# Kernel tuning notes

Measured on AMD Instinct MI355X. Metric: run time of the kernel, lower is better.

Reference implementation:

```python
import jax, jax.numpy as jnp
import numpy as np

B, C, H, W = 8, 64, 64, 64
PROJ = 8


def setup_inputs() -> dict:
    key = jax.random.key(0)
    ks = jax.random.split(key, 8)
    inp = {
        "query_x": jax.random.normal(ks[0], (B, C, H, W), dtype=jnp.float32),
        "ref_x": jax.random.normal(ks[1], (B, C, H, W), dtype=jnp.float32),
        # 1x1 conv weights stored as [out_ch, in_ch] (kernel_size=1)
        "wq": jax.random.normal(ks[2], (PROJ, C), dtype=jnp.float32) * 0.05,
        "bq": jnp.zeros((PROJ,), dtype=jnp.float32),
        "wk": jax.random.normal(ks[3], (PROJ, C), dtype=jnp.float32) * 0.05,
        "bk": jnp.zeros((PROJ,), dtype=jnp.float32),
        "wv": jax.random.normal(ks[4], (C, C), dtype=jnp.float32) * 0.05,
        "bv": jnp.zeros((C,), dtype=jnp.float32),
    }
    return inp


def reference(query_x, ref_x, wq, bq, wk, bk, wv, bv):
    b, c, h, w = ref_x.shape
    n = h * w
    # 1x1 conv projections, flattened to [B, ch, HW]
    q = (jnp.einsum("oc,bchw->bohw", wq, query_x) + bq[None, :, None, None]).reshape(b, PROJ, n)
    k = (jnp.einsum("oc,bchw->bohw", wk, ref_x) + bk[None, :, None, None]).reshape(b, PROJ, n)
    v = (jnp.einsum("oc,bchw->bohw", wv, ref_x) + bv[None, :, None, None]).reshape(b, c, n)
    # energy[b, j(ref), i(query)] = sum_p k[b,p,j] * q[b,p,i]  (unscaled)
    energy = jnp.einsum("bpj,bpi->bji", k, q)
    attention = jax.nn.softmax(energy, axis=-1)
    # z = bmm(v, attention^T): z[b,c,j] = sum_i v[b,c,i] * attention[b,j,i]
    z = jnp.einsum("bci,bji->bcj", v, attention).reshape(b, c, h, w)
    return query_x + z
```

## Files before the change

### kernel.cpp

```cpp
#include <hip/hip_runtime.h>
#include <hip/hip_bf16.h>

#define B_ 8
#define C_ 64
#define N_ 4096
#define ITERS 16

typedef __attribute__((ext_vector_type(4))) short bf16x4;
typedef __attribute__((ext_vector_type(8))) short bf16x8;
typedef __attribute__((ext_vector_type(2))) float f32x2;
typedef __attribute__((ext_vector_type(4))) float f32x4;

static __device__ inline ushort f2bf(float x) {
    union { float f; unsigned u; } c; c.f = x;
    return (ushort)((c.u + 0x7FFFu + ((c.u >> 16) & 1u)) >> 16);
}
static __device__ inline float exp2fast(float x) {
#if __has_builtin(__builtin_amdgcn_exp2f)
    return __builtin_amdgcn_exp2f(x);
#else
    return exp2f(x);
#endif
}

#if __has_builtin(__builtin_amdgcn_mfma_f32_16x16x16bf16_1k)
static __device__ inline f32x4 mfma16(bf16x4 a, bf16x4 b, f32x4 c) {
    return __builtin_amdgcn_mfma_f32_16x16x16bf16_1k(a, b, c, 0, 0, 0);
}
#else
static __device__ inline f32x4 mfma16(bf16x4 a, bf16x4 b, f32x4 c) {
    bf16x8 a8 = (bf16x8){a[0], a[1], a[2], a[3], 0, 0, 0, 0};
    bf16x8 b8 = (bf16x8){b[0], b[1], b[2], b[3], 0, 0, 0, 0};
    return __builtin_amdgcn_mfma_f32_16x16x32_bf16(a8, b8, c, 0, 0, 0);
}
#endif
static __device__ inline f32x4 mfma32(bf16x8 a, bf16x8 b, f32x4 c) {
    return __builtin_amdgcn_mfma_f32_16x16x32_bf16(a, b, c, 0, 0, 0);
}

static __device__ inline void gload16(const void* g, void* l) {
#if __has_builtin(__builtin_amdgcn_global_load_lds)
    __builtin_amdgcn_global_load_lds(
        (const __attribute__((address_space(1))) void*)g,
        (__attribute__((address_space(3))) void*)l, 16, 0, 0);
#else
    const int lane = threadIdx.x & 63;
    *(int4*)((char*)l + lane * 16) = *(const int4*)((const char*)g + lane * 16);
#endif
}

__global__ __launch_bounds__(256) void proj_kernel(
    const float* __restrict__ qx, const float* __restrict__ rx,
    const float* __restrict__ wq, const float* __restrict__ bq,
    const float* __restrict__ wk, const float* __restrict__ bk,
    const float* __restrict__ wv, const float* __restrict__ bv,
    ushort* __restrict__ qb, ushort* __restrict__ kb, ushort* __restrict__ vt2)
{
    const int og  = blockIdx.y;
    const int gid = blockIdx.x * 256 + threadIdx.x;
    const int b   = gid >> 12;
    const int i   = gid & (N_ - 1);

    const int t  = i >> 5;
    const int lo = i & 7;
    const int hi = (i >> 3) & 3;
    ushort* tb = vt2 + ((size_t)(b * 128 + t)) * 2048;

    if (og == 0) {
        const float* xp = qx + (size_t)b * C_ * N_ + i;
        float a[8];
#pragma unroll
        for (int p = 0; p < 8; ++p) a[p] = bq[p];
        for (int c = 0; c < C_; ++c) {
            const float x = xp[(size_t)c * N_];
#pragma unroll
            for (int p = 0; p < 8; ++p) a[p] = fmaf(wq[p * C_ + c], x, a[p]);
        }
        ushort u8[8];
#pragma unroll
        for (int p = 0; p < 8; ++p) u8[p] = f2bf(a[p]);
        int4 r;
        r.x = (int)(u8[0] | ((unsigned)u8[1] << 16));
        r.y = (int)(u8[2] | ((unsigned)u8[3] << 16));
        r.z = (int)(u8[4] | ((unsigned)u8[5] << 16));
        r.w = (int)(u8[6] | ((unsigned)u8[7] << 16));
        *(int4*)(qb + (size_t)gid * 8) = r;
    } else if (og == 1) {
        const float* xp = rx + (size_t)b * C_ * N_ + i;
        float ak[8], av[32];
#pragma unroll
        for (int p = 0; p < 8; ++p) ak[p] = bk[p];
#pragma unroll
        for (int p = 0; p < 32; ++p) av[p] = bv[p];
        for (int c = 0; c < C_; ++c) {
            const float x = xp[(size_t)c * N_];
#pragma unroll
            for (int p = 0; p < 8; ++p) ak[p] = fmaf(wk[p * C_ + c], x, ak[p]);
#pragma unroll
            for (int p = 0; p < 32; ++p) av[p] = fmaf(wv[p * C_ + c], x, av[p]);
        }
        const float s = 1.44269504088896340736f;
        ushort u8[8];
#pragma unroll
        for (int p = 0; p < 8; ++p) u8[p] = f2bf(ak[p] * s);
        int4 r;
        r.x = (int)(u8[0] | ((unsigned)u8[1] << 16));
        r.y = (int)(u8[2] | ((unsigned)u8[3] << 16));
        r.z = (int)(u8[4] | ((unsigned)u8[5] << 16));
        r.w = (int)(u8[6] | ((unsigned)u8[7] << 16));
        *(int4*)(kb + (size_t)gid * 8) = r;
#pragma unroll
        for (int p = 0; p < 32; ++p)
            tb[p * 32 + ((hi ^ ((p >> 1) & 3)) << 3) + lo] = f2bf(av[p]);
    } else {
        const float* xp = rx + (size_t)b * C_ * N_ + i;
        float av[32];
#pragma unroll
        for (int p = 0; p < 32; ++p) av[p] = bv[32 + p];
        for (int c = 0; c < C_; ++c) {
            const float x = xp[(size_t)c * N_];
#pragma unroll
            for (int p = 0; p < 32; ++p)
                av[p] = fmaf(wv[(32 + p) * C_ + c], x, av[p]);
        }
#pragma unroll
        for (int p = 0; p < 32; ++p) {
            const int c = 32 + p;
            tb[c * 32 + ((hi ^ ((c >> 1) & 3)) << 3) + lo] = f2bf(av[p]);
        }
    }
}

__global__ __launch_bounds__(512, 4) void attn_kernel(
    const ushort* __restrict__ qb, const ushort* __restrict__ kb,
    const ushort* __restrict__ vt2, const float* __restrict__ qx,
    float* __restrict__ out)
{
    __shared__ __align__(16) char smem[65536];
    float* o_lds    = (float*)smem;
    float* lsum_lds = (float*)(smem + 2 * 64 * 68 * 4);

    const int tid  = threadIdx.x;
    const int ig   = tid >> 6;
    const int lane = tid & 63;
    const int cc   = lane & 15;
    const int g    = lane >> 4;
    const int b    = blockIdx.x;
    const int j0   = blockIdx.y * 64;

    bf16x4 bk[4];
#pragma unroll
    for (int jb = 0; jb < 4; ++jb) bk[jb] = (bf16x4){0, 0, 0, 0};
    if (g < 2) {
#pragma unroll
        for (int jb = 0; jb < 4; ++jb)
            bk[jb] = *(const bf16x4*)(kb + ((size_t)b * N_ + j0 + jb * 16 + cc) * 8 + g * 4);
    }

    const int qperm = 8 * (cc >> 2) + (cc & 3);
    const ushort* qptr = qb + ((size_t)b * N_ + (size_t)ig * (N_ / 8) + qperm) * 8 + g * 4;

    const char* vsl = (const char*)vt2 + ((size_t)(b * 128 + ig * 16)) * 4096 + lane * 16;
    char* lds0 = smem + ig * 8192;

    f32x4 acc[4][4];
#pragma unroll
    for (int jb = 0; jb < 4; ++jb)
#pragma unroll
        for (int ct = 0; ct < 4; ++ct) acc[jb][ct] = (f32x4){0.f, 0.f, 0.f, 0.f};
    f32x2 ls2[4];
#pragma unroll
    for (int jb = 0; jb < 4; ++jb) ls2[jb] = (f32x2){0.f, 0.f};
    const f32x4 zero4 = (f32x4){0.f, 0.f, 0.f, 0.f};

    const int rb = cc * 32 + ((g ^ ((cc >> 1) & 3)) << 3);

    bf16x4 qa0 = *(const bf16x4*)(qptr);
    bf16x4 qa1 = *(const bf16x4*)(qptr + 32);
    gload16(vsl, lds0);
    gload16(vsl + 1024, lds0 + 1024);
    gload16(vsl + 2048, lds0 + 2048);
    gload16(vsl + 3072, lds0 + 3072);
    bf16x4 qb0 = *(const bf16x4*)(qptr + 256);
    bf16x4 qb1 = *(const bf16x4*)(qptr + 256 + 32);
    asm volatile("s_waitcnt vmcnt(0)" ::: "memory");
    __builtin_amdgcn_sched_barrier(0);

#define HALF_ITER(Q0, Q1, RBOFF, WBOFF, IT)                                    \
    {                                                                          \
        asm volatile("s_waitcnt vmcnt(2)" ::: "memory");                       \
        __builtin_amdgcn_sched_barrier(0);                                     \
        const ushort* vtile = (const ushort*)(lds0 + (RBOFF));                 \
        bf16x8 av0 = *(const bf16x8*)(vtile + rb);                             \
        bf16x8 av1 = *(const bf16x8*)(vtile + rb + 512);                       \
        bf16x8 av2 = *(const bf16x8*)(vtile + rb + 1024);                      \
        bf16x8 av3 = *(const bf16x8*)(vtile + rb + 1536);                      \
        {                                                                      \
            const int nxt = ((IT) + 1) & (ITERS - 1);                          \
            const char* s = vsl + (size_t)nxt * 4096;                          \
            char* dd = lds0 + (WBOFF);                                         \
            gload16(s, dd);                                                    \
            gload16(s + 1024, dd + 1024);                                      \
            gload16(s + 2048, dd + 2048);                                      \
            gload16(s + 3072, dd + 3072);                                      \
        }                                                                      \
        __builtin_amdgcn_sched_barrier(0);                                     \
        _Pragma("unroll")                                                      \
        for (int jb = 0; jb < 4; ++jb) {                                       \
            f32x4 e0 = mfma16(Q0, bk[jb], zero4);                              \
            f32x4 e1 = mfma16(Q1, bk[jb], zero4);                              \
            float p0 = exp2fast(e0[0]), p1 = exp2fast(e0[1]);                  \
            float p2 = exp2fast(e0[2]), p3 = exp2fast(e0[3]);                  \
            float p4 = exp2fast(e1[0]), p5 = exp2fast(e1[1]);                  \
            float p6 = exp2fast(e1[2]), p7 = exp2fast(e1[3]);                  \
            union { bf16x8 v; __hip_bfloat162 h[4]; } pu;                      \
            pu.h[0] = __float22bfloat162_rn(make_float2(p0, p1));              \
            pu.h[1] = __float22bfloat162_rn(make_float2(p2, p3));              \
            pu.h[2] = __float22bfloat162_rn(make_float2(p4, p5));              \
            pu.h[3] = __float22bfloat162_rn(make_float2(p6, p7));              \
            f32x2 sA = (f32x2){p0, p1} + (f32x2){p2, p3};                      \
            f32x2 sB = (f32x2){p4, p5} + (f32x2){p6, p7};                      \
            ls2[jb] += sA + sB;                                                \
            acc[jb][0] = mfma32(av0, pu.v, acc[jb][0]);                        \
            acc[jb][1] = mfma32(av1, pu.v, acc[jb][1]);                        \
            acc[jb][2] = mfma32(av2, pu.v, acc[jb][2]);                        \
            acc[jb][3] = mfma32(av3, pu.v, acc[jb][3]);                        \
        }                                                                      \
        {                                                                      \
            const int nq = ((IT) + 2) & (ITERS - 1);                           \
            const ushort* qp = qptr + (size_t)nq * 256;                        \
            Q0 = *(const bf16x4*)(qp);                                         \
            Q1 = *(const bf16x4*)(qp + 32);                                    \
        }                                                                      \
    }

#pragma unroll 1
    for (int d = 0; d < ITERS / 2; ++d) {
        const int it0 = 2 * d;
        HALF_ITER(qa0, qa1, 0, 4096, it0);
        HALF_ITER(qb0, qb1, 4096, 0, it0 + 1);
    }
#undef HALF_ITER

    float ls[4];
#pragma unroll
    for (int jb = 0; jb < 4; ++jb) {
        ls[jb] = ls2[jb][0] + ls2[jb][1];
        ls[jb] += __shfl_xor(ls[jb], 16, 64);
        ls[jb] += __shfl_xor(ls[jb], 32, 64);
    }

    __syncthreads();
    {
        const int phme = ig >> 1;
        float* od = o_lds + (ig & 1) * (64 * 68);
        float* ld = lsum_lds + (ig & 1) * 64;
#pragma unroll 1
        for (int ph = 0; ph < 4; ++ph) {
            if (phme == ph) {
                if (ph == 0) {
#pragma unroll
                    for (int jb = 0; jb < 4; ++jb)
#pragma unroll
                        for (int ct = 0; ct < 4; ++ct)
#pragma unroll
                            for (int r = 0; r < 4; ++r)
                                od[(ct * 16 + 4 * g + r) * 68 + jb * 16 + cc] = acc[jb][ct][r];
                    if (g == 0) {
#pragma unroll
                        for (int jb = 0; jb < 4; ++jb) ld[jb * 16 + cc] = ls[jb];
                    }
                } else {
#pragma unroll
                    for (int jb = 0; jb < 4; ++jb)
#pragma unroll
                        for (int ct = 0; ct < 4; ++ct)
#pragma unroll
                            for (int r = 0; r < 4; ++r)
                                od[(ct * 16 + 4 * g + r) * 68 + jb * 16 + cc] += acc[jb][ct][r];
                    if (g == 0) {
#pragma unroll
                        for (int jb = 0; jb < 4; ++jb) ld[jb * 16 + cc] += ls[jb];
                    }
                }
            }
            __syncthreads();
        }
    }

    const int ec = tid >> 3;
    const int ej = (tid & 7) * 8;
    const float* xp = qx  + ((size_t)b * C_ + ec) * N_ + j0 + ej;
    float*       op = out + ((size_t)b * C_ + ec) * N_ + j0 + ej;
    float4 x0 = *(const float4*)xp;
    float4 x1 = *(const float4*)(xp + 4);
    float rr[8];
#pragma unroll
    for (int t = 0; t < 8; ++t) {
        const float num = o_lds[ec * 68 + ej + t] + o_lds[64 * 68 + ec * 68 + ej + t];
        const float den = lsum_lds[ej + t] + lsum_lds[64 + ej + t];
        rr[t] = num / den;
    }
    float4 r0 = make_float4(x0.x + rr[0], x0.y + rr[1], x0.z + rr[2], x0.w + rr[3]);
    float4 r1 = make_float4(x1.x + rr[4], x1.y + rr[5], x1.z + rr[6], x1.w + rr[7]);
    *(float4*)op       = r0;
    *(float4*)(op + 4) = r1;
}

extern "C" void kernel_launch(void* const* d_in, const int* in_sizes, int n_in,
                              void* d_out, int out_size, void* d_ws, size_t ws_size,
                              hipStream_t stream) {
    const float* qx = (const float*)d_in[0];
    const float* rx = (const float*)d_in[1];
    const float* wq = (const float*)d_in[2];
    const float* bq = (const float*)d_in[3];
    const float* wk = (const float*)d_in[4];
    const float* bk = (const float*)d_in[5];
    const float* wv = (const float*)d_in[6];
    const float* bv = (const float*)d_in[7];
    float* out = (float*)d_out;

    ushort* qb  = (ushort*)d_ws;
    ushort* kb  = qb + (size_t)B_ * N_ * 8;
    ushort* vt2 = kb + (size_t)B_ * N_ * 8;

    proj_kernel<<<dim3((B_ * N_) / 256, 3), 256, 0, stream>>>(
        qx, rx, wq, bq, wk, bk, wv, bv, qb, kb, vt2);

    attn_kernel<<<dim3(B_, N_ / 64), 512, 0, stream>>>(qb, kb, vt2, qx, out);
}
```

Before: 52.57 us.

## Load V fragments directly from global into registers, dropping LDS staging

The projection kernel now writes V in an MFMA-fragment-ready layout, so each lane can read its bf16x8 A-operands for the attention kernel straight from global memory. This removes the global_load_lds double-buffered staging, the manual vmcnt waits, the sched barriers and the LDS reads. It also shrinks shared memory to just the reduction buffers, which may allow more resident blocks. In exchange, register-prefetched global loads depend on the compiler to hide latency, without explicit pipeline control.

```diff
diff --git a/kernel.cpp b/kernel.cpp
--- a/kernel.cpp
+++ b/kernel.cpp
@@ -8,7 +8,6 @@
 
 typedef __attribute__((ext_vector_type(4))) short bf16x4;
 typedef __attribute__((ext_vector_type(8))) short bf16x8;
-typedef __attribute__((ext_vector_type(2))) float f32x2;
 typedef __attribute__((ext_vector_type(4))) float f32x4;
 
 static __device__ inline ushort f2bf(float x) {
@@ -36,17 +35,6 @@
 #endif
 static __device__ inline f32x4 mfma32(bf16x8 a, bf16x8 b, f32x4 c) {
     return __builtin_amdgcn_mfma_f32_16x16x32_bf16(a, b, c, 0, 0, 0);
-}
-
-static __device__ inline void gload16(const void* g, void* l) {
-#if __has_builtin(__builtin_amdgcn_global_load_lds)
-    __builtin_amdgcn_global_load_lds(
-        (const __attribute__((address_space(1))) void*)g,
-        (__attribute__((address_space(3))) void*)l, 16, 0, 0);
-#else
-    const int lane = threadIdx.x & 63;
-    *(int4*)((char*)l + lane * 16) = *(const int4*)((const char*)g + lane * 16);
-#endif
 }
 
 __global__ __launch_bounds__(256) void proj_kernel(
@@ -62,9 +50,10 @@
     const int i   = gid & (N_ - 1);
 
     const int t  = i >> 5;
-    const int lo = i & 7;
-    const int hi = (i >> 3) & 3;
-    ushort* tb = vt2 + ((size_t)(b * 128 + t)) * 2048;
+    const int il = i & 31;
+    const int fl = (il >> 3) * 16;
+    const int fe = il & 7;
+    ushort* tb = vt2 + (size_t)(b * 128 + t) * 2048;
 
     if (og == 0) {
         const float* xp = qx + (size_t)b * C_ * N_ + i;
@@ -111,7 +100,7 @@
         *(int4*)(kb + (size_t)gid * 8) = r;
 #pragma unroll
         for (int p = 0; p < 32; ++p)
-            tb[p * 32 + ((hi ^ ((p >> 1) & 3)) << 3) + lo] = f2bf(av[p]);
+            tb[(p >> 4) * 512 + (fl + (p & 15)) * 8 + fe] = f2bf(av[p]);
     } else {
         const float* xp = rx + (size_t)b * C_ * N_ + i;
         float av[32];
@@ -126,7 +115,7 @@
 #pragma unroll
         for (int p = 0; p < 32; ++p) {
             const int c = 32 + p;
-            tb[c * 32 + ((hi ^ ((c >> 1) & 3)) << 3) + lo] = f2bf(av[p]);
+            tb[(c >> 4) * 512 + (fl + (c & 15)) * 8 + fe] = f2bf(av[p]);
         }
     }
 }
@@ -136,9 +125,8 @@
     const ushort* __restrict__ vt2, const float* __restrict__ qx,
     float* __restrict__ out)
 {
-    __shared__ __align__(16) char smem[65536];
-    float* o_lds    = (float*)smem;
-    float* lsum_lds = (float*)(smem + 2 * 64 * 68 * 4);
+    __shared__ float o_lds[2 * 64 * 68];
+    __shared__ float lsum_lds[2 * 64];
 
     const int tid  = threadIdx.x;
     const int ig   = tid >> 6;
@@ -160,92 +148,61 @@
     const int qperm = 8 * (cc >> 2) + (cc & 3);
     const ushort* qptr = qb + ((size_t)b * N_ + (size_t)ig * (N_ / 8) + qperm) * 8 + g * 4;
 
-    const char* vsl = (const char*)vt2 + ((size_t)(b * 128 + ig * 16)) * 4096 + lane * 16;
-    char* lds0 = smem + ig * 8192;
+    const ushort* vbase = vt2 + (size_t)(b * 128 + ig * 16) * 2048 + lane * 8;
 
     f32x4 acc[4][4];
 #pragma unroll
     for (int jb = 0; jb < 4; ++jb)
 #pragma unroll
         for (int ct = 0; ct < 4; ++ct) acc[jb][ct] = (f32x4){0.f, 0.f, 0.f, 0.f};
-    f32x2 ls2[4];
-#pragma unroll
-    for (int jb = 0; jb < 4; ++jb) ls2[jb] = (f32x2){0.f, 0.f};
+    float ls[4] = {0.f, 0.f, 0.f, 0.f};
     const f32x4 zero4 = (f32x4){0.f, 0.f, 0.f, 0.f};
 
-    const int rb = cc * 32 + ((g ^ ((cc >> 1) & 3)) << 3);
-
+    bf16x8 av0 = *(const bf16x8*)(vbase);
+    bf16x8 av1 = *(const bf16x8*)(vbase + 512);
+    bf16x8 av2 = *(const bf16x8*)(vbase + 1024);
+    bf16x8 av3 = *(const bf16x8*)(vbase + 1536);
     bf16x4 qa0 = *(const bf16x4*)(qptr);
     bf16x4 qa1 = *(const bf16x4*)(qptr + 32);
-    gload16(vsl, lds0);
-    gload16(vsl + 1024, lds0 + 1024);
-    gload16(vsl + 2048, lds0 + 2048);
-    gload16(vsl + 3072, lds0 + 3072);
-    bf16x4 qb0 = *(const bf16x4*)(qptr + 256);
-    bf16x4 qb1 = *(const bf16x4*)(qptr + 256 + 32);
-    asm volatile("s_waitcnt vmcnt(0)" ::: "memory");
-    __builtin_amdgcn_sched_barrier(0);
-
-#define HALF_ITER(Q0, Q1, RBOFF, WBOFF, IT)                                    \
-    {                                                                          \
-        asm volatile("s_waitcnt vmcnt(2)" ::: "memory");                       \
-        __builtin_amdgcn_sched_barrier(0);                                     \
-        const ushort* vtile = (const ushort*)(lds0 + (RBOFF));                 \
-        bf16x8 av0 = *(const bf16x8*)(vtile + rb);                             \
-        bf16x8 av1 = *(const bf16x8*)(vtile + rb + 512);                       \
-        bf16x8 av2 = *(const bf16x8*)(vtile + rb + 1024);                      \
-        bf16x8 av3 = *(const bf16x8*)(vtile + rb + 1536);                      \
-        {                                                                      \
-            const int nxt = ((IT) + 1) & (ITERS - 1);                          \
-            const char* s = vsl + (size_t)nxt * 4096;                          \
-            char* dd = lds0 + (WBOFF);                                         \
-            gload16(s, dd);                                                    \
-            gload16(s + 1024, dd + 1024);                                      \
-            gload16(s + 2048, dd + 2048);                                      \
-            gload16(s + 3072, dd + 3072);                                      \
-        }                                                                      \
-        __builtin_amdgcn_sched_barrier(0);                                     \
-        _Pragma("unroll")                                                      \
-        for (int jb = 0; jb < 4; ++jb) {                                       \
-            f32x4 e0 = mfma16(Q0, bk[jb], zero4);                              \
-            f32x4 e1 = mfma16(Q1, bk[jb], zero4);                              \
-            float p0 = exp2fast(e0[0]), p1 = exp2fast(e0[1]);                  \
-            float p2 = exp2fast(e0[2]), p3 = exp2fast(e0[3]);                  \
-            float p4 = exp2fast(e1[0]), p5 = exp2fast(e1[1]);                  \
-            float p6 = exp2fast(e1[2]), p7 = exp2fast(e1[3]);                  \
-            union { bf16x8 v; __hip_bfloat162 h[4]; } pu;                      \
-            pu.h[0] = __float22bfloat162_rn(make_float2(p0, p1));              \
-            pu.h[1] = __float22bfloat162_rn(make_float2(p2, p3));              \
-            pu.h[2] = __float22bfloat162_rn(make_float2(p4, p5));              \
-            pu.h[3] = __float22bfloat162_rn(make_float2(p6, p7));              \
-            f32x2 sA = (f32x2){p0, p1} + (f32x2){p2, p3};                      \
-            f32x2 sB = (f32x2){p4, p5} + (f32x2){p6, p7};                      \
-            ls2[jb] += sA + sB;                                                \
-            acc[jb][0] = mfma32(av0, pu.v, acc[jb][0]);                        \
-            acc[jb][1] = mfma32(av1, pu.v, acc[jb][1]);                        \
-            acc[jb][2] = mfma32(av2, pu.v, acc[jb][2]);                        \
-            acc[jb][3] = mfma32(av3, pu.v, acc[jb][3]);                        \
-        }                                                                      \
-        {                                                                      \
-            const int nq = ((IT) + 2) & (ITERS - 1);                           \
-            const ushort* qp = qptr + (size_t)nq * 256;                        \
-            Q0 = *(const bf16x4*)(qp);                                         \
-            Q1 = *(const bf16x4*)(qp + 32);                                    \
-        }                                                                      \
-    }
-
-#pragma unroll 1
-    for (int d = 0; d < ITERS / 2; ++d) {
-        const int it0 = 2 * d;
-        HALF_ITER(qa0, qa1, 0, 4096, it0);
-        HALF_ITER(qb0, qb1, 4096, 0, it0 + 1);
-    }
-#undef HALF_ITER
-
-    float ls[4];
+
+#pragma unroll 2
+    for (int it = 0; it < ITERS; ++it) {
+        const int nxt = (it + 1) & (ITERS - 1);
+        const ushort* vp = vbase + nxt * 2048;
+        bf16x8 nv0 = *(const bf16x8*)(vp);
+        bf16x8 nv1 = *(const bf16x8*)(vp + 512);
+        bf16x8 nv2 = *(const bf16x8*)(vp + 1024);
+        bf16x8 nv3 = *(const bf16x8*)(vp + 1536);
+        const ushort* qp = qptr + (size_t)nxt * 256;
+        bf16x4 nq0 = *(const bf16x4*)(qp);
+        bf16x4 nq1 = *(const bf16x4*)(qp + 32);
+
+#pragma unroll
+        for (int jb = 0; jb < 4; ++jb) {
+            f32x4 e0 = mfma16(qa0, bk[jb], zero4);
+            f32x4 e1 = mfma16(qa1, bk[jb], zero4);
+            float p0 = exp2fast(e0[0]), p1 = exp2fast(e0[1]);
+            float p2 = exp2fast(e0[2]), p3 = exp2fast(e0[3]);
+            float p4 = exp2fast(e1[0]), p5 = exp2fast(e1[1]);
+            float p6 = exp2fast(e1[2]), p7 = exp2fast(e1[3]);
+            union { bf16x8 v; __hip_bfloat162 h[4]; } pu;
+            pu.h[0] = __float22bfloat162_rn(make_float2(p0, p1));
+            pu.h[1] = __float22bfloat162_rn(make_float2(p2, p3));
+            pu.h[2] = __float22bfloat162_rn(make_float2(p4, p5));
+            pu.h[3] = __float22bfloat162_rn(make_float2(p6, p7));
+            ls[jb] += ((p0 + p1) + (p2 + p3)) + ((p4 + p5) + (p6 + p7));
+            acc[jb][0] = mfma32(av0, pu.v, acc[jb][0]);
+            acc[jb][1] = mfma32(av1, pu.v, acc[jb][1]);
+            acc[jb][2] = mfma32(av2, pu.v, acc[jb][2]);
+            acc[jb][3] = mfma32(av3, pu.v, acc[jb][3]);
+        }
+
+        av0 = nv0; av1 = nv1; av2 = nv2; av3 = nv3;
+        qa0 = nq0; qa1 = nq1;
+    }
+
 #pragma unroll
     for (int jb = 0; jb < 4; ++jb) {
-        ls[jb] = ls2[jb][0] + ls2[jb][1];
         ls[jb] += __shfl_xor(ls[jb], 16, 64);
         ls[jb] += __shfl_xor(ls[jb], 32, 64);
     }
```

Result: slower. 60.98 us (+16.0%).
